# Kernel tuning notes

Hardware: AMD Instinct MI355X
Metric: run time of the kernel (lower is better)

The kernel has to match this reference:

```python
import jax, jax.numpy as jnp
import numpy as np

B, M, T, F_IN, H = 16, 512, 64, 128, 128


def _gru_layer(x, wih, whh, bih, bhh):
    # x: [B, T, H_in]; torch nn.GRU gate math, single layer, h0 = 0
    Hh = whh.shape[1]

    def step(h_prev, x_t):
        gi = x_t @ wih.T + bih          # [B, 3H]
        gh = h_prev @ whh.T + bhh       # [B, 3H]
        i_r, i_z, i_n = jnp.split(gi, 3, axis=-1)
        h_r, h_z, h_n = jnp.split(gh, 3, axis=-1)
        r = jax.nn.sigmoid(i_r + h_r)
        z = jax.nn.sigmoid(i_z + h_z)
        n = jnp.tanh(i_n + r * h_n)
        h_new = (1.0 - z) * n + z * h_prev
        return h_new, h_new

    h0 = jnp.zeros((x.shape[0], Hh), x.dtype)
    _, ys = jax.lax.scan(step, h0, jnp.swapaxes(x, 0, 1))  # [T, B, H]
    return jnp.swapaxes(ys, 0, 1)                          # [B, T, H]


def setup_inputs() -> dict:
    key = jax.random.key(0)
    ks = jax.random.split(key, 12)
    s = 0.05

    def w(k, shape):
        return jax.random.normal(k, shape, jnp.float32) * s

    return {
        "X": jax.random.normal(ks[0], (B, M, T, F_IN), jnp.float32),
        "C": jax.random.normal(ks[1], (B, M, T), jnp.float32),
        "h_target": jax.random.normal(ks[2], (B, T, H), jnp.float32),
        "distance": jax.random.uniform(ks[3], (M,), jnp.float32),
        "lin_w": w(ks[4], (H, F_IN)), "lin_b": jnp.zeros((H,), jnp.float32),
        "mlp_w1": w(ks[5], (H, 2 * H)), "mlp_b1": jnp.zeros((H,), jnp.float32),
        "mlp_w2": w(ks[6], (1, H)), "mlp_b2": jnp.zeros((1,), jnp.float32),
        "lin2_w": w(ks[7], (1, 3)), "lin2_b": jnp.zeros((1,), jnp.float32),
        "gru_wih0": w(ks[8], (3 * H, H)), "gru_whh0": w(ks[9], (3 * H, H)),
        "gru_bih0": jnp.zeros((3 * H,), jnp.float32), "gru_bhh0": jnp.zeros((3 * H,), jnp.float32),
        "gru_wih1": w(ks[10], (3 * H, H)), "gru_whh1": w(ks[11], (3 * H, H)),
        "gru_bih1": jnp.zeros((3 * H,), jnp.float32), "gru_bhh1": jnp.zeros((3 * H,), jnp.float32),
    }


def reference(X, C, h_target, distance,
              lin_w, lin_b, mlp_w1, mlp_b1, mlp_w2, mlp_b2,
              lin2_w, lin2_b,
              gru_wih0, gru_whh0, gru_bih0, gru_bhh0,
              gru_wih1, gru_whh1, gru_bih1, gru_bhh1):
    # h: [B, M, T, H]
    h = jnp.einsum('bmtf,hf->bmth', X, lin_w) + lin_b
    # broadcast h_target over message dim M: [B, 1, T, H] -> [B, M, T, H]
    ht = jnp.broadcast_to(h_target[:, None, :, :], h.shape)
    cat = jnp.concatenate([ht, h], axis=-1)                    # [B, M, T, 2H]
    mlp_h = jax.nn.relu(jnp.einsum('bmtf,hf->bmth', cat, mlp_w1) + mlp_b1)
    w_msg = jnp.einsum('bmth,oh->bmto', mlp_h, mlp_w2) + mlp_b2  # [B, M, T, 1]
    # distance broadcast: [1, M, 1, 1] -> [B, M, T, 1]
    dist = jnp.broadcast_to(distance[None, :, None, None], w_msg.shape)
    coef = jnp.concatenate([C[..., None], dist, w_msg], axis=-1)  # [B, M, T, 3]
    learned_w = coef @ lin2_w.T + lin2_b                          # [B, M, T, 1]
    h_agg = jnp.sum(h * learned_w, axis=1)                        # [B, T, H]
    # 2-layer GRU (eval mode: no dropout)
    out0 = _gru_layer(h_agg, gru_wih0, gru_whh0, gru_bih0, gru_bhh0)
    out1 = _gru_layer(out0, gru_wih1, gru_whh1, gru_bih1, gru_bhh1)
    return out1
```

## Files before the change

kernel.cpp:

```cpp
#include <hip/hip_runtime.h>
#include <math.h>

#define NB 16
#define NM 512
#define NT 64
#define NF 128
#define NH 128
#define PAD4 132

typedef short short8 __attribute__((ext_vector_type(8)));
typedef float floatx4 __attribute__((ext_vector_type(4)));

static __device__ __forceinline__ unsigned short f2b(float f) {
  union { float f; unsigned u; } v; v.f = f;
  unsigned r = v.u + 0x7fff + ((v.u >> 16) & 1);
  return (unsigned short)(r >> 16);
}

__global__ __launch_bounds__(128) void prep_kernel(
    const float* __restrict__ lin_w, const float* __restrict__ mlp_w1,
    const float* __restrict__ lin_b, const float* __restrict__ mlp_b1,
    unsigned short* __restrict__ WxFrag, float* __restrict__ linT,
    float* __restrict__ ubase)
{
  const int tid = threadIdx.x;
  if (blockIdx.x < 128) {
    const int i = blockIdx.x;
    __shared__ float sw[128];
    __shared__ float rb[128];
    sw[tid] = mlp_w1[i * 256 + 128 + tid];
    __syncthreads();
    float s = 0.f;
#pragma unroll 16
    for (int k = 0; k < 128; k++) s += sw[k] * lin_w[k * 128 + tid];
    {
      const int it = i >> 4, col = i & 15;
      const int f = tid;
      const int kc = f >> 5, quad = (f >> 3) & 3, jj = f & 7;
      WxFrag[((it * 4 + kc) * 64 + quad * 16 + col) * 8 + jj] = f2b(s);
    }
    rb[tid] = sw[tid] * lin_b[tid];
    __syncthreads();
    if (tid == 0) {
      float s2 = 0.f;
      for (int k = 0; k < 128; k++) s2 += rb[k];
      ubase[i] = mlp_b1[i] + s2;
    }
  } else {
    const int f = blockIdx.x - 128;
    linT[f * 128 + tid] = lin_w[tid * 128 + f];
  }
}

static __device__ __forceinline__ void tpose_tile(
    const float* __restrict__ in, float* __restrict__ outT,
    int R, int C, int S, int tileIdx)
{
  __shared__ float tile[32][33];
  const int tilesC = C >> 5;
  const int tr = tileIdx / tilesC, tc = tileIdx % tilesC;
  const int x = threadIdx.x & 31, y = threadIdx.x >> 5;
#pragma unroll
  for (int yy = y; yy < 32; yy += 8)
    tile[yy][x] = in[(size_t)(tr * 32 + yy) * S + tc * 32 + x];
  __syncthreads();
#pragma unroll
  for (int yy = y; yy < 32; yy += 8)
    outT[(size_t)(tc * 32 + yy) * R + tr * 32 + x] = tile[x][yy];
}

__global__ __launch_bounds__(256) void tpose_kernel(
    const float* __restrict__ wih0, const float* __restrict__ whh0,
    const float* __restrict__ wih1, const float* __restrict__ whh1,
    const float* __restrict__ mlp_w1,
    float* __restrict__ wih0T, float* __restrict__ whh0T,
    float* __restrict__ wih1T, float* __restrict__ whh1T,
    float* __restrict__ W1aT)
{
  const int b = blockIdx.x;
  if (b < 48)        tpose_tile(wih0,   wih0T, 384, 128, 128, b);
  else if (b < 96)   tpose_tile(whh0,   whh0T, 384, 128, 128, b - 48);
  else if (b < 144)  tpose_tile(wih1,   wih1T, 384, 128, 128, b - 96);
  else if (b < 192)  tpose_tile(whh1,   whh1T, 384, 128, 128, b - 144);
  else               tpose_tile(mlp_w1, W1aT,  128, 128, 256, b - 192);
}

__global__ __launch_bounds__(128) void u_kernel(
    const float* __restrict__ h_target, const float* __restrict__ W1aT,
    const float* __restrict__ ubase, float* __restrict__ u_out)
{
  const int bt = blockIdx.x, i = threadIdx.x;
  __shared__ float sht[128];
  sht[i] = h_target[bt * 128 + i];
  __syncthreads();
  float u = ubase[i];
#pragma unroll 16
  for (int k = 0; k < 128; k++) u += W1aT[k * 128 + i] * sht[k];
  u_out[bt * 128 + i] = u;
}

__global__ __launch_bounds__(256, 4) void pass1_kernel(
    const float* __restrict__ X, const float* __restrict__ C,
    const float* __restrict__ dist,
    const unsigned short* __restrict__ WxFrag, const float* __restrict__ u_g,
    const float* __restrict__ mlp_w2, const float* __restrict__ mlp_b2,
    const float* __restrict__ lin2_w, const float* __restrict__ lin2_b,
    float* __restrict__ part, float* __restrict__ partls)
{
  const int blk = blockIdx.x;
  const int g = blk & 7, bt = blk >> 3;
  const int b = bt >> 6, t = bt & 63;
  const int tid = threadIdx.x;

  __shared__ float xs[64 * PAD4];
  __shared__ float u_sh[128], w2_sh[128], lw_sh[64];
  __shared__ float red[2][128];
  __shared__ float red_ls;

  const float* Xbase = X + (((size_t)(b * NM + g * 64)) * NT + t) * NF;
#pragma unroll
  for (int p = 0; p < 8; p++) {
    int idx = p * 256 + tid;
    int row = idx >> 5, c4 = idx & 31;
    float4 xv = *(const float4*)(Xbase + (size_t)row * NT * NF + c4 * 4);
    *(float4*)&xs[row * PAD4 + c4 * 4] = xv;
  }
  if (tid < 128) { u_sh[tid] = u_g[bt * 128 + tid]; w2_sh[tid] = mlp_w2[tid]; }
  __syncthreads();

  const int w = tid >> 6, lane = tid & 63;
  const int col = lane & 15, quad = lane >> 4;
  short8 afr[4];
#pragma unroll
  for (int kc = 0; kc < 4; kc++) {
    const float* src = &xs[(w * 16 + col) * PAD4 + kc * 32 + quad * 8];
    short8 a;
#pragma unroll
    for (int jv = 0; jv < 8; jv++) a[jv] = (short)f2b(src[jv]);
    afr[kc] = a;
  }
  floatx4 acc[8];
#pragma unroll
  for (int it = 0; it < 8; it++) acc[it] = {0.f, 0.f, 0.f, 0.f};
#pragma unroll
  for (int it = 0; it < 8; it++) {
#pragma unroll
    for (int kc = 0; kc < 4; kc++) {
      short8 bfr = *(const short8*)&WxFrag[((it * 4 + kc) * 64 + lane) * 8];
      acc[it] = __builtin_amdgcn_mfma_f32_16x16x32_bf16(afr[kc], bfr, acc[it], 0, 0, 0);
    }
  }

  float w2l[8], ul[8];
#pragma unroll
  for (int it = 0; it < 8; it++) { w2l[it] = w2_sh[it * 16 + col]; ul[it] = u_sh[it * 16 + col]; }
  float vsum[4];
#pragma unroll
  for (int r = 0; r < 4; r++) {
    float v = 0.f;
#pragma unroll
    for (int it = 0; it < 8; it++) {
      float s = acc[it][r] + ul[it];
      v += w2l[it] * fmaxf(s, 0.f);
    }
    v += __shfl_xor(v, 1, 64);
    v += __shfl_xor(v, 2, 64);
    v += __shfl_xor(v, 4, 64);
    v += __shfl_xor(v, 8, 64);
    vsum[r] = v;
  }
  if (col == 0) {
    const float c0 = lin2_w[0], c1 = lin2_w[1], c2 = lin2_w[2];
    const float lb2 = lin2_b[0], mb2 = mlp_b2[0];
#pragma unroll
    for (int r = 0; r < 4; r++) {
      int ml = w * 16 + quad * 4 + r;
      int m = g * 64 + ml;
      float wmsg = vsum[r] + mb2;
      lw_sh[ml] = C[((size_t)b * NM + m) * NT + t] * c0 + dist[m] * c1 + wmsg * c2 + lb2;
    }
  }
  __syncthreads();

  const int f = tid & 127, half = tid >> 7;
  float xa = 0.f;
#pragma unroll 8
  for (int mm = half * 32; mm < half * 32 + 32; mm++)
    xa += lw_sh[mm] * xs[mm * PAD4 + f];
  red[half][f] = xa;
  if (tid < 64) {
    float v = lw_sh[tid];
    v += __shfl_xor(v, 1, 64);
    v += __shfl_xor(v, 2, 64);
    v += __shfl_xor(v, 4, 64);
    v += __shfl_xor(v, 8, 64);
    v += __shfl_xor(v, 16, 64);
    v += __shfl_xor(v, 32, 64);
    if (tid == 0) red_ls = v;
  }
  __syncthreads();
  if (tid < 128) part[(size_t)blk * 128 + tid] = red[0][tid] + red[1][tid];
  if (tid == 128) partls[blk] = red_ls;
}

__global__ __launch_bounds__(384) void reduce_kernel(
    const float* __restrict__ part, const float* __restrict__ partls,
    const float* __restrict__ linT, const float* __restrict__ lin_b,
    const float* __restrict__ wih0T, const float* __restrict__ bih0,
    float* __restrict__ gi0)
{
  const int bt = blockIdx.x, j = threadIdx.x;
  __shared__ float sxa[128], shh[128];
  __shared__ float sls;
  if (j < 128) {
    float s = 0.f;
#pragma unroll
    for (int g2 = 0; g2 < 8; g2++) s += part[((size_t)bt * 8 + g2) * 128 + j];
    sxa[j] = s;
  }
  if (j == 128) {
    float s = 0.f;
#pragma unroll
    for (int g2 = 0; g2 < 8; g2++) s += partls[bt * 8 + g2];
    sls = s;
  }
  __syncthreads();
  if (j < 128) {
    float hv = sls * lin_b[j];
#pragma unroll 8
    for (int f2 = 0; f2 < 128; f2++) hv += linT[f2 * 128 + j] * sxa[f2];
    shh[j] = hv;
  }
  __syncthreads();
  float gacc = bih0[j];
#pragma unroll 16
  for (int k = 0; k < 128; k++) gacc += wih0T[k * 384 + j] * shh[k];
  gi0[(size_t)bt * 384 + j] = gacc;
}

__global__ __launch_bounds__(384, 2) void gi_kernel(
    const float* __restrict__ xin, const float* __restrict__ wihT,
    const float* __restrict__ bih, float* __restrict__ gi)
{
  __shared__ __align__(16) float xr[128];
  const int bt = blockIdx.x, j = threadIdx.x;
  if (j < 128) xr[j] = xin[bt * 128 + j];
  __syncthreads();
  float a0 = 0.f, a1 = 0.f, a2 = 0.f, a3 = 0.f;
#pragma unroll 8
  for (int k = 0; k < 128; k += 4) {
    a0 += wihT[(k    ) * 384 + j] * xr[k];
    a1 += wihT[(k + 1) * 384 + j] * xr[k + 1];
    a2 += wihT[(k + 2) * 384 + j] * xr[k + 2];
    a3 += wihT[(k + 3) * 384 + j] * xr[k + 3];
  }
  gi[(size_t)bt * 384 + j] = (a0 + a1) + (a2 + a3) + bih[j];
}

__global__ __launch_bounds__(384, 1) void gru_layer_kernel(
    const float* __restrict__ gi, const float* __restrict__ whhT,
    const float* __restrict__ bhh, float* __restrict__ out)
{
  const int b = blockIdx.x, j = threadIdx.x;
  __shared__ float sgi[64 * 384];
  __shared__ float hs[128], ghs[384];

  const float4* gsrc = (const float4*)(gi + (size_t)b * 64 * 384);
  float4* gdst = (float4*)sgi;
#pragma unroll
  for (int p = 0; p < 16; p++) gdst[p * 384 + j] = gsrc[p * 384 + j];

  float wreg[128];
#pragma unroll
  for (int k = 0; k < 128; k++) wreg[k] = whhT[k * 384 + j];
  const float bh = bhh[j];
  if (j < 128) hs[j] = 0.f;
  __syncthreads();

  for (int t = 0; t < NT; t++) {
    float a0 = 0.f, a1 = 0.f, a2 = 0.f, a3 = 0.f;
    const float4* h4 = (const float4*)hs;
#pragma unroll
    for (int k = 0; k < 32; k++) {
      float4 hv = h4[k];
      a0 += wreg[4 * k]     * hv.x;
      a1 += wreg[4 * k + 1] * hv.y;
      a2 += wreg[4 * k + 2] * hv.z;
      a3 += wreg[4 * k + 3] * hv.w;
    }
    ghs[j] = (a0 + a1) + (a2 + a3) + bh;
    __syncthreads();
    if (j < 128) {
      const float* gt = &sgi[t * 384];
      const float hprev = hs[j];
      const float r = 1.f / (1.f + expf(-(gt[j] + ghs[j])));
      const float z = 1.f / (1.f + expf(-(gt[128 + j] + ghs[128 + j])));
      const float n = tanhf(gt[256 + j] + r * ghs[256 + j]);
      const float hnew = (1.f - z) * n + z * hprev;
      hs[j] = hnew;
      out[((size_t)b * NT + t) * 128 + j] = hnew;
    }
    __syncthreads();
  }
}

extern "C" void kernel_launch(void* const* d_in, const int* in_sizes, int n_in,
                              void* d_out, int out_size, void* d_ws, size_t ws_size,
                              hipStream_t stream)
{
  const float* X        = (const float*)d_in[0];
  const float* C        = (const float*)d_in[1];
  const float* h_target = (const float*)d_in[2];
  const float* distance = (const float*)d_in[3];
  const float* lin_w    = (const float*)d_in[4];
  const float* lin_b    = (const float*)d_in[5];
  const float* mlp_w1   = (const float*)d_in[6];
  const float* mlp_b1   = (const float*)d_in[7];
  const float* mlp_w2   = (const float*)d_in[8];
  const float* mlp_b2   = (const float*)d_in[9];
  const float* lin2_w   = (const float*)d_in[10];
  const float* lin2_b   = (const float*)d_in[11];
  const float* wih0     = (const float*)d_in[12];
  const float* whh0     = (const float*)d_in[13];
  const float* bih0     = (const float*)d_in[14];
  const float* bhh0     = (const float*)d_in[15];
  const float* wih1     = (const float*)d_in[16];
  const float* whh1     = (const float*)d_in[17];
  const float* bih1     = (const float*)d_in[18];
  const float* bhh1     = (const float*)d_in[19];
  float* out = (float*)d_out;

  float* ws = (float*)d_ws;
  unsigned short* WxFrag = (unsigned short*)ws;
  float* linT   = ws + 8192;
  float* u_buf  = ws + 24576;
  float* part   = ws + 155648;
  float* partls = ws + 1204224;
  float* gi     = ws + 1212416;
  float* out0   = ws + 1605632;
  float* W1aT   = ws + 1736704;
  float* wih0T  = ws + 1753088;
  float* whh0T  = ws + 1802240;
  float* wih1T  = ws + 1851392;
  float* whh1T  = ws + 1900544;
  float* ubase  = ws + 1949696;

  prep_kernel<<<256, 128, 0, stream>>>(lin_w, mlp_w1, lin_b, mlp_b1, WxFrag, linT, ubase);
  tpose_kernel<<<208, 256, 0, stream>>>(wih0, whh0, wih1, whh1, mlp_w1,
      wih0T, whh0T, wih1T, whh1T, W1aT);
  u_kernel<<<NB * NT, 128, 0, stream>>>(h_target, W1aT, ubase, u_buf);
  pass1_kernel<<<NB * NT * 8, 256, 0, stream>>>(X, C, distance, WxFrag, u_buf,
      mlp_w2, mlp_b2, lin2_w, lin2_b, part, partls);
  reduce_kernel<<<NB * NT, 384, 0, stream>>>(part, partls, linT, lin_b, wih0T, bih0, gi);
  gru_layer_kernel<<<NB, 384, 0, stream>>>(gi, whh0T, bhh0, out0);
  gi_kernel<<<NB * NT, 384, 0, stream>>>(out0, wih1T, bih1, gi);
  gru_layer_kernel<<<NB, 384, 0, stream>>>(gi, whh1T, bhh1, out);
}
```

Baseline: 619.3 us.

## Split GRU recurrence across two K halves, merge setup kernels, add nontemporal hints

The GRU layer kernel now runs 768 threads per block, with each half computing a partial recurrent matvec over 64 of the 128 hidden inputs. The partials are summed in shared memory, which halves the serial per-step dot-product length. The two setup kernels (prep and transpose) are merged into one launch, and the lin_w transpose uses a tiled path. Nontemporal loads and stores are applied to the X stream and the partial-sum buffer to reduce cache pollution. The GRU gets more shared-memory traffic and relies on 768-thread blocks holding 64 registers of weights per thread.

New measurement: 559.6 us. -9.6%, faster.

```diff
diff --git a/kernel.cpp b/kernel.cpp
--- a/kernel.cpp
+++ b/kernel.cpp
@@ -10,6 +10,7 @@
 
 typedef short short8 __attribute__((ext_vector_type(8)));
 typedef float floatx4 __attribute__((ext_vector_type(4)));
+typedef float f4 __attribute__((ext_vector_type(4)));
 
 static __device__ __forceinline__ unsigned short f2b(float f) {
   union { float f; unsigned u; } v; v.f = f;
@@ -17,29 +18,52 @@
   return (unsigned short)(r >> 16);
 }
 
-__global__ __launch_bounds__(128) void prep_kernel(
+static __device__ __forceinline__ void tpose_tile(
+    const float* __restrict__ in, float* __restrict__ outT,
+    int R, int C, int S, int tileIdx)
+{
+  __shared__ float tile[32][33];
+  const int tilesC = C >> 5;
+  const int tr = tileIdx / tilesC, tc = tileIdx % tilesC;
+  const int x = threadIdx.x & 31, y = threadIdx.x >> 5;
+#pragma unroll
+  for (int yy = y; yy < 32; yy += 8)
+    tile[yy][x] = in[(size_t)(tr * 32 + yy) * S + tc * 32 + x];
+  __syncthreads();
+#pragma unroll
+  for (int yy = y; yy < 32; yy += 8)
+    outT[(size_t)(tc * 32 + yy) * R + tr * 32 + x] = tile[x][yy];
+}
+
+__global__ __launch_bounds__(256) void setup_kernel(
     const float* __restrict__ lin_w, const float* __restrict__ mlp_w1,
     const float* __restrict__ lin_b, const float* __restrict__ mlp_b1,
+    const float* __restrict__ wih0, const float* __restrict__ whh0,
+    const float* __restrict__ wih1, const float* __restrict__ whh1,
     unsigned short* __restrict__ WxFrag, float* __restrict__ linT,
-    float* __restrict__ ubase)
-{
+    float* __restrict__ ubase,
+    float* __restrict__ wih0T, float* __restrict__ whh0T,
+    float* __restrict__ wih1T, float* __restrict__ whh1T,
+    float* __restrict__ W1aT)
+{
+  const int blk = blockIdx.x;
   const int tid = threadIdx.x;
-  if (blockIdx.x < 128) {
-    const int i = blockIdx.x;
+  if (blk < 128) {
+    const int i = blk;
     __shared__ float sw[128];
     __shared__ float rb[128];
-    sw[tid] = mlp_w1[i * 256 + 128 + tid];
+    if (tid < 128) sw[tid] = mlp_w1[i * 256 + 128 + tid];
     __syncthreads();
-    float s = 0.f;
+    if (tid < 128) {
+      float s = 0.f;
 #pragma unroll 16
-    for (int k = 0; k < 128; k++) s += sw[k] * lin_w[k * 128 + tid];
-    {
+      for (int k = 0; k < 128; k++) s += sw[k] * lin_w[k * 128 + tid];
       const int it = i >> 4, col = i & 15;
       const int f = tid;
       const int kc = f >> 5, quad = (f >> 3) & 3, jj = f & 7;
       WxFrag[((it * 4 + kc) * 64 + quad * 16 + col) * 8 + jj] = f2b(s);
-    }
-    rb[tid] = sw[tid] * lin_b[tid];
+      rb[tid] = sw[tid] * lin_b[tid];
+    }
     __syncthreads();
     if (tid == 0) {
       float s2 = 0.f;
@@ -47,42 +71,14 @@
       ubase[i] = mlp_b1[i] + s2;
     }
   } else {
-    const int f = blockIdx.x - 128;
-    linT[f * 128 + tid] = lin_w[tid * 128 + f];
-  }
-}
-
-static __device__ __forceinline__ void tpose_tile(
-    const float* __restrict__ in, float* __restrict__ outT,
-    int R, int C, int S, int tileIdx)
-{
-  __shared__ float tile[32][33];
-  const int tilesC = C >> 5;
-  const int tr = tileIdx / tilesC, tc = tileIdx % tilesC;
-  const int x = threadIdx.x & 31, y = threadIdx.x >> 5;
-#pragma unroll
-  for (int yy = y; yy < 32; yy += 8)
-    tile[yy][x] = in[(size_t)(tr * 32 + yy) * S + tc * 32 + x];
-  __syncthreads();
-#pragma unroll
-  for (int yy = y; yy < 32; yy += 8)
-    outT[(size_t)(tc * 32 + yy) * R + tr * 32 + x] = tile[x][yy];
-}
-
-__global__ __launch_bounds__(256) void tpose_kernel(
-    const float* __restrict__ wih0, const float* __restrict__ whh0,
-    const float* __restrict__ wih1, const float* __restrict__ whh1,
-    const float* __restrict__ mlp_w1,
-    float* __restrict__ wih0T, float* __restrict__ whh0T,
-    float* __restrict__ wih1T, float* __restrict__ whh1T,
-    float* __restrict__ W1aT)
-{
-  const int b = blockIdx.x;
-  if (b < 48)        tpose_tile(wih0,   wih0T, 384, 128, 128, b);
-  else if (b < 96)   tpose_tile(whh0,   whh0T, 384, 128, 128, b - 48);
-  else if (b < 144)  tpose_tile(wih1,   wih1T, 384, 128, 128, b - 96);
-  else if (b < 192)  tpose_tile(whh1,   whh1T, 384, 128, 128, b - 144);
-  else               tpose_tile(mlp_w1, W1aT,  128, 128, 256, b - 192);
+    const int c = blk - 128;
+    if (c < 48)        tpose_tile(wih0,   wih0T, 384, 128, 128, c);
+    else if (c < 96)   tpose_tile(whh0,   whh0T, 384, 128, 128, c - 48);
+    else if (c < 144)  tpose_tile(wih1,   wih1T, 384, 128, 128, c - 96);
+    else if (c < 192)  tpose_tile(whh1,   whh1T, 384, 128, 128, c - 144);
+    else if (c < 208)  tpose_tile(mlp_w1, W1aT,  128, 128, 256, c - 192);
+    else               tpose_tile(lin_w,  linT,  128, 128, 128, c - 208);
+  }
 }
 
 __global__ __launch_bounds__(128) void u_kernel(
@@ -122,8 +118,8 @@
   for (int p = 0; p < 8; p++) {
     int idx = p * 256 + tid;
     int row = idx >> 5, c4 = idx & 31;
-    float4 xv = *(const float4*)(Xbase + (size_t)row * NT * NF + c4 * 4);
-    *(float4*)&xs[row * PAD4 + c4 * 4] = xv;
+    f4 xv = __builtin_nontemporal_load((const f4*)(Xbase + (size_t)row * NT * NF + c4 * 4));
+    *(f4*)&xs[row * PAD4 + c4 * 4] = xv;
   }
   if (tid < 128) { u_sh[tid] = u_g[bt * 128 + tid]; w2_sh[tid] = mlp_w2[tid]; }
   __syncthreads();
@@ -199,7 +195,8 @@
     if (tid == 0) red_ls = v;
   }
   __syncthreads();
-  if (tid < 128) part[(size_t)blk * 128 + tid] = red[0][tid] + red[1][tid];
+  if (tid < 128) __builtin_nontemporal_store(red[0][tid] + red[1][tid],
+                                             &part[(size_t)blk * 128 + tid]);
   if (tid == 128) partls[blk] = red_ls;
 }
 
@@ -215,7 +212,8 @@
   if (j < 128) {
     float s = 0.f;
 #pragma unroll
-    for (int g2 = 0; g2 < 8; g2++) s += part[((size_t)bt * 8 + g2) * 128 + j];
+    for (int g2 = 0; g2 < 8; g2++)
+      s += __builtin_nontemporal_load(&part[((size_t)bt * 8 + g2) * 128 + j]);
     sxa[j] = s;
   }
   if (j == 128) {
@@ -257,48 +255,55 @@
   gi[(size_t)bt * 384 + j] = (a0 + a1) + (a2 + a3) + bih[j];
 }
 
-__global__ __launch_bounds__(384, 1) void gru_layer_kernel(
+__global__ __launch_bounds__(768) void gru_layer_kernel(
     const float* __restrict__ gi, const float* __restrict__ whhT,
     const float* __restrict__ bhh, float* __restrict__ out)
 {
-  const int b = blockIdx.x, j = threadIdx.x;
+  const int b = blockIdx.x, tid = threadIdx.x;
+  const int kh = (tid >= 384) ? 1 : 0;
+  const int j  = tid - kh * 384;
+
   __shared__ float sgi[64 * 384];
-  __shared__ float hs[128], ghs[384];
+  __shared__ float hs[128];
+  __shared__ float pg[2][384];
 
   const float4* gsrc = (const float4*)(gi + (size_t)b * 64 * 384);
   float4* gdst = (float4*)sgi;
 #pragma unroll
-  for (int p = 0; p < 16; p++) gdst[p * 384 + j] = gsrc[p * 384 + j];
-
-  float wreg[128];
-#pragma unroll
-  for (int k = 0; k < 128; k++) wreg[k] = whhT[k * 384 + j];
-  const float bh = bhh[j];
-  if (j < 128) hs[j] = 0.f;
+  for (int p = 0; p < 8; p++) gdst[p * 768 + tid] = gsrc[p * 768 + tid];
+
+  float wreg[64];
+#pragma unroll
+  for (int k = 0; k < 64; k++) wreg[k] = whhT[(kh * 64 + k) * 384 + j];
+  const float bh = (kh == 0) ? bhh[j] : 0.f;
+  if (tid < 128) hs[tid] = 0.f;
   __syncthreads();
 
   for (int t = 0; t < NT; t++) {
+    const float4* h4 = ((const float4*)hs) + kh * 16;
     float a0 = 0.f, a1 = 0.f, a2 = 0.f, a3 = 0.f;
-    const float4* h4 = (const float4*)hs;
-#pragma unroll
-    for (int k = 0; k < 32; k++) {
+#pragma unroll
+    for (int k = 0; k < 16; k++) {
       float4 hv = h4[k];
       a0 += wreg[4 * k]     * hv.x;
       a1 += wreg[4 * k + 1] * hv.y;
       a2 += wreg[4 * k + 2] * hv.z;
       a3 += wreg[4 * k + 3] * hv.w;
     }
-    ghs[j] = (a0 + a1) + (a2 + a3) + bh;
+    pg[kh][j] = (a0 + a1) + (a2 + a3) + bh;
     __syncthreads();
-    if (j < 128) {
+    if (tid < 128) {
       const float* gt = &sgi[t * 384];
-      const float hprev = hs[j];
-      const float r = 1.f / (1.f + expf(-(gt[j] + ghs[j])));
-      const float z = 1.f / (1.f + expf(-(gt[128 + j] + ghs[128 + j])));
-      const float n = tanhf(gt[256 + j] + r * ghs[256 + j]);
+      const float ghr = pg[0][tid]       + pg[1][tid];
+      const float ghz = pg[0][tid + 128] + pg[1][tid + 128];
+      const float ghn = pg[0][tid + 256] + pg[1][tid + 256];
+      const float hprev = hs[tid];
+      const float r = 1.f / (1.f + expf(-(gt[tid] + ghr)));
+      const float z = 1.f / (1.f + expf(-(gt[tid + 128] + ghz)));
+      const float n = tanhf(gt[tid + 256] + r * ghn);
       const float hnew = (1.f - z) * n + z * hprev;
-      hs[j] = hnew;
-      out[((size_t)b * NT + t) * 128 + j] = hnew;
+      hs[tid] = hnew;
+      out[((size_t)b * NT + t) * 128 + tid] = hnew;
     }
     __syncthreads();
   }
@@ -345,14 +350,14 @@
   float* whh1T  = ws + 1900544;
   float* ubase  = ws + 1949696;
 
-  prep_kernel<<<256, 128, 0, stream>>>(lin_w, mlp_w1, lin_b, mlp_b1, WxFrag, linT, ubase);
-  tpose_kernel<<<208, 256, 0, stream>>>(wih0, whh0, wih1, whh1, mlp_w1,
-      wih0T, whh0T, wih1T, whh1T, W1aT);
+  setup_kernel<<<352, 256, 0, stream>>>(lin_w, mlp_w1, lin_b, mlp_b1,
+      wih0, whh0, wih1, whh1,
+      WxFrag, linT, ubase, wih0T, whh0T, wih1T, whh1T, W1aT);
   u_kernel<<<NB * NT, 128, 0, stream>>>(h_target, W1aT, ubase, u_buf);
   pass1_kernel<<<NB * NT * 8, 256, 0, stream>>>(X, C, distance, WxFrag, u_buf,
       mlp_w2, mlp_b2, lin2_w, lin2_b, part, partls);
   reduce_kernel<<<NB * NT, 384, 0, stream>>>(part, partls, linT, lin_b, wih0T, bih0, gi);
-  gru_layer_kernel<<<NB, 384, 0, stream>>>(gi, whh0T, bhh0, out0);
+  gru_layer_kernel<<<NB, 768, 0, stream>>>(gi, whh0T, bhh0, out0);
   gi_kernel<<<NB * NT, 384, 0, stream>>>(out0, wih1T, bih1, gi);
-  gru_layer_kernel<<<NB, 384, 0, stream>>>(gi, whh1T, bhh1, out);
-}
+  gru_layer_kernel<<<NB, 768, 0, stream>>>(gi, whh1T, bhh1, out);
+}
```
